# Kernel tuning notes

Measured on AMD Instinct MI355X. Metric: run time of the kernel, lower is better.

Reference implementation:

```python
import jax, jax.numpy as jnp
import numpy as np

GRID_H = 64
GRID_W = 64


def make_grid(h, w):
    # torch.meshgrid([arange(h), arange(w)], indexing='xy') -> shape (w, h);
    # grid[i, j] = (j + 0.5, i + 0.5). With h == w == 64 this is square.
    gx, gy = jnp.meshgrid(jnp.arange(h, dtype=jnp.float32),
                          jnp.arange(w, dtype=jnp.float32), indexing='xy')
    return jnp.stack([gx, gy], axis=-1) + 0.5  # (w, h, 2)


def setup_inputs() -> dict:
    key = jax.random.key(0)
    k1, k2 = jax.random.split(key)
    x = jax.random.normal(k1, (4, 128, 64, 64), dtype=jnp.float32)
    y = jax.random.normal(k2, (4, 128, 64, 64), dtype=jnp.float32)
    return {"x": x, "y": y}


def reference(x, y):
    b, c, hx, wx = x.shape
    _, _, hy, wy = y.shape
    scale = c ** (-0.5)
    grids = make_grid(GRID_H, GRID_W)[:hy, :wy].reshape(-1, 2)  # (hy*wy, 2)

    x_ = x.reshape(b, c, hx * wx)
    y_ = y.reshape(b, c, hy * wy)
    # (b, q, k) attention over all key pixels
    attn = jax.nn.softmax(jnp.einsum('bcq,bck->bqk', x_, y_) * scale, axis=-1)
    uv = jnp.einsum('bqk,kt->bqt', attn, grids)  # (b, hx*wx, 2)
    uv = uv.reshape(b, hx, wx, 2)
    # normalize to [-1, 1]
    norm = jnp.asarray([wy, hy], dtype=uv.dtype)
    uv = uv / norm * 2.0 - 1.0
    return uv
```

## Files before the change

kernel.cpp:

```cpp
#include <hip/hip_runtime.h>
#include <math.h>

typedef __attribute__((ext_vector_type(8))) _Float16 f16x8;
typedef __attribute__((ext_vector_type(4))) float f32x4;

#define NPIX 4096
#define C_DIM 128
#define SCALE 0.08838834764831845f

#define WS_NEED ((size_t)4 << 20)

__global__ __launch_bounds__(256) void conv_y(const float* __restrict__ y,
                                              char* __restrict__ ws)
{
    __shared__ float T[32][132];
    const int wg  = blockIdx.x;
    const int xcd = wg & 7;
    const int b   = xcd >> 1;
    const int sl  = ((xcd & 1) << 6) | (wg >> 3);
    const int k0  = sl * 32;
    const int t   = threadIdx.x;

    {
        const int c = t >> 1, half = t & 1;
        const float* srow = y + ((size_t)b * C_DIM + c) * NPIX + k0 + half * 16;
        float4 rv[4];
        #pragma unroll
        for (int u = 0; u < 4; ++u) rv[u] = *(const float4*)(srow + u * 4);
        #pragma unroll
        for (int u = 0; u < 4; ++u) {
            T[half * 16 + u * 4 + 0][c] = rv[u].x;
            T[half * 16 + u * 4 + 1][c] = rv[u].y;
            T[half * 16 + u * 4 + 2][c] = rv[u].z;
            T[half * 16 + u * 4 + 3][c] = rv[u].w;
        }
    }
    __syncthreads();

    char* panel = ws + (size_t)b * (NPIX * 256);
    const int k = t >> 3, g2 = t & 7;
    f16x8 v0, v1;
    #pragma unroll
    for (int m = 0; m < 8; ++m) {
        v0[m] = (_Float16)T[k][g2 * 16 + m];
        v1[m] = (_Float16)T[k][g2 * 16 + 8 + m];
    }
    const int key = k0 + k, s = key & 7;
    char* drow = panel + (size_t)key * 256;
    *(f16x8*)(drow + (((2 * g2)     ^ s) << 4)) = v0;
    *(f16x8*)(drow + (((2 * g2 + 1) ^ s) << 4)) = v1;
}

__global__ __launch_bounds__(256, 2) void uv_main(const char* __restrict__ ws,
                                                  const float* __restrict__ x,
                                                  float* __restrict__ out)
{
    __shared__ __align__(16) char Ys[2][32768];

    const int t = threadIdx.x, w = t >> 6, l = t & 63;
    const int n16 = l & 15, quad = l >> 4;
    const int wg  = blockIdx.x;
    const int xcd = wg & 7;
    const int b   = xcd >> 1;
    const int qt  = ((xcd & 1) << 6) | (wg >> 3);
    const int q0  = qt * 32;

    f16x8 bh[4][2], bl[4][2];
    {
        const float* xb = x + (size_t)b * C_DIM * NPIX + q0 + n16;
        #pragma unroll
        for (int cc = 0; cc < 4; ++cc)
            #pragma unroll
            for (int qg = 0; qg < 2; ++qg) {
                f16x8 hh, ll;
                #pragma unroll
                for (int j = 0; j < 8; ++j) {
                    const float f = xb[(size_t)(cc * 32 + quad * 8 + j) * NPIX + qg * 16] * SCALE;
                    const _Float16 fh = (_Float16)f;
                    hh[j] = fh;
                    ll[j] = (_Float16)(f - (float)fh);
                }
                bh[cc][qg] = hh;
                bl[cc][qg] = ll;
            }
    }

    const char* panel = ws + (size_t)b * (NPIX * 256);

    int aoff[2][4];
    #pragma unroll
    for (int mt = 0; mt < 2; ++mt)
        #pragma unroll
        for (int cc = 0; cc < 4; ++cc)
            aoff[mt][cc] = (mt * 64 + w * 16 + n16) * 256 + (((cc * 4 + quad) ^ (n16 & 7)) << 4);

    float gxr[4];
    #pragma unroll
    for (int r = 0; r < 4; ++r) gxr[r] = (float)(w * 16 + quad * 4 + r) + 0.5f;

    float den[2] = {0.f, 0.f}, nu[2] = {0.f, 0.f}, nv[2] = {0.f, 0.f};

    #pragma unroll
    for (int h = 0; h < 2; ++h)
        #pragma unroll
        for (int i = 0; i < 4; ++i) {
            const int off = (h * 64 + w * 16 + i * 4) * 256;
            __builtin_amdgcn_global_load_lds(
                (const __attribute__((address_space(1))) void*)(panel + off + l * 16),
                (__attribute__((address_space(3))) void*)(&Ys[0][off]), 16, 0, 0);
        }

    #pragma unroll 2
    for (int kt = 0; kt < 32; ++kt) {
        const int cur = kt & 1;
        __syncthreads();

        if (kt < 31) {
            const char* gt = panel + (size_t)(kt + 1) * 32768;
            #pragma unroll
            for (int h = 0; h < 2; ++h)
                #pragma unroll
                for (int i = 0; i < 4; ++i) {
                    const int off = (h * 64 + w * 16 + i * 4) * 256;
                    __builtin_amdgcn_global_load_lds(
                        (const __attribute__((address_space(1))) void*)(gt + off + l * 16),
                        (__attribute__((address_space(3))) void*)(&Ys[cur ^ 1][off]), 16, 0, 0);
                }
        }

        f32x4 acc[2][2];
        #pragma unroll
        for (int mt = 0; mt < 2; ++mt)
            #pragma unroll
            for (int qg = 0; qg < 2; ++qg) acc[mt][qg] = (f32x4){0.f, 0.f, 0.f, 0.f};

        #pragma unroll
        for (int cc = 0; cc < 4; ++cc) {
            const f16x8 A0 = *(const f16x8*)(&Ys[cur][aoff[0][cc]]);
            const f16x8 A1 = *(const f16x8*)(&Ys[cur][aoff[1][cc]]);
            #pragma unroll
            for (int qg = 0; qg < 2; ++qg) {
                acc[0][qg] = __builtin_amdgcn_mfma_f32_16x16x32_f16(A0, bh[cc][qg], acc[0][qg], 0, 0, 0);
                acc[0][qg] = __builtin_amdgcn_mfma_f32_16x16x32_f16(A0, bl[cc][qg], acc[0][qg], 0, 0, 0);
                acc[1][qg] = __builtin_amdgcn_mfma_f32_16x16x32_f16(A1, bh[cc][qg], acc[1][qg], 0, 0, 0);
                acc[1][qg] = __builtin_amdgcn_mfma_f32_16x16x32_f16(A1, bl[cc][qg], acc[1][qg], 0, 0, 0);
            }
        }

        #pragma unroll
        for (int qg = 0; qg < 2; ++qg) {
            float d = 0.f, u = 0.f, v = 0.f;
            #pragma unroll
            for (int mt = 0; mt < 2; ++mt) {
                const float gy = (float)(kt * 2 + mt) + 0.5f;
                #pragma unroll
                for (int r = 0; r < 4; ++r) {
                    const float p = __expf(acc[mt][qg][r]);
                    d += p;
                    u += p * gxr[r];
                    v += p * gy;
                }
            }
            den[qg] += d; nu[qg] += u; nv[qg] += v;
        }
    }

    #pragma unroll
    for (int qg = 0; qg < 2; ++qg) {
        #pragma unroll
        for (int mk = 16; mk <= 32; mk <<= 1) {
            den[qg] += __shfl_xor(den[qg], mk);
            nu[qg]  += __shfl_xor(nu[qg],  mk);
            nv[qg]  += __shfl_xor(nv[qg],  mk);
        }
    }
    __syncthreads();
    float* red = (float*)&Ys[0][0];
    if (quad == 0) {
        #pragma unroll
        for (int qg = 0; qg < 2; ++qg) {
            const int base = (w * 32 + qg * 16 + n16) * 3;
            red[base + 0] = den[qg];
            red[base + 1] = nu[qg];
            red[base + 2] = nv[qg];
        }
    }
    __syncthreads();
    if (t < 32) {
        float d = 0.f, u = 0.f, v = 0.f;
        #pragma unroll
        for (int ww = 0; ww < 4; ++ww) {
            d += red[(ww * 32 + t) * 3 + 0];
            u += red[(ww * 32 + t) * 3 + 1];
            v += red[(ww * 32 + t) * 3 + 2];
        }
        const float inv = 1.0f / d;
        *(float2*)(out + ((size_t)b * NPIX + q0 + t) * 2) =
            make_float2(u * inv * 0.03125f - 1.0f, v * inv * 0.03125f - 1.0f);
    }
}

__global__ __launch_bounds__(256, 2) void uv_attn_kernel(
    const float* __restrict__ x, const float* __restrict__ y, float* __restrict__ out)
{
    __shared__ float Xs[C_DIM][32];
    __shared__ float Ysf[64][128];
    const int tid = threadIdx.x;
    const int wgid = blockIdx.x;
    const int xcd = wgid & 7;
    const int b = xcd & 3;
    const int q0 = (((xcd >> 2) << 6) | (wgid >> 3)) * 32;
    const float* xb = x + (size_t)b * C_DIM * NPIX + q0;
    {
        const int cr = tid >> 3;
        const int cc = (tid & 7) << 2;
        #pragma unroll
        for (int i = 0; i < 4; ++i) {
            float4 v = *(const float4*)(xb + (size_t)(cr + (i << 5)) * NPIX + cc);
            v.x *= SCALE; v.y *= SCALE; v.z *= SCALE; v.w *= SCALE;
            *(float4*)(&Xs[cr + (i << 5)][cc]) = v;
        }
    }
    const int rg = tid >> 4;
    const int lane16 = tid & 15;
    const int r0 = rg << 1;
    const int col0 = lane16 << 3;
    float gxv[8];
    #pragma unroll
    for (int j2 = 0; j2 < 8; ++j2) gxv[j2] = (float)((col0 & 63) + j2) + 0.5f;
    const float gyb = (float)(lane16 >> 3) + 0.5f;
    float m_run[2] = {-INFINITY, -INFINITY};
    float den[2] = {0.f, 0.f}, nu[2] = {0.f, 0.f}, nv[2] = {0.f, 0.f};
    const int yr = tid >> 5;
    const int yc = (tid & 31) << 2;
    const float* ybase = y + (size_t)b * C_DIM * NPIX;
    for (int kt = 0; kt < 32; ++kt) {
        float S[2][8];
        #pragma unroll
        for (int r = 0; r < 2; ++r)
            #pragma unroll
            for (int j2 = 0; j2 < 8; ++j2) S[r][j2] = 0.f;
        #pragma unroll
        for (int cb = 0; cb < 2; ++cb) {
            __syncthreads();
            const float* yt = ybase + (size_t)(cb << 6) * NPIX + kt * 128;
            #pragma unroll
            for (int i = 0; i < 8; ++i)
                *(float4*)(&Ysf[yr + (i << 3)][yc]) =
                    *(const float4*)(yt + (size_t)(yr + (i << 3)) * NPIX + yc);
            __syncthreads();
            const int cbase = cb << 6;
            #pragma unroll 16
            for (int c = 0; c < 64; ++c) {
                const float2 xa = *(const float2*)(&Xs[cbase + c][r0]);
                const float4 ya = *(const float4*)(&Ysf[c][col0]);
                const float4 yb4 = *(const float4*)(&Ysf[c][col0 + 4]);
                S[0][0] += xa.x * ya.x;  S[0][1] += xa.x * ya.y;
                S[0][2] += xa.x * ya.z;  S[0][3] += xa.x * ya.w;
                S[0][4] += xa.x * yb4.x; S[0][5] += xa.x * yb4.y;
                S[0][6] += xa.x * yb4.z; S[0][7] += xa.x * yb4.w;
                S[1][0] += xa.y * ya.x;  S[1][1] += xa.y * ya.y;
                S[1][2] += xa.y * ya.z;  S[1][3] += xa.y * ya.w;
                S[1][4] += xa.y * yb4.x; S[1][5] += xa.y * yb4.y;
                S[1][6] += xa.y * yb4.z; S[1][7] += xa.y * yb4.w;
            }
        }
        const float gy = gyb + 2.0f * (float)kt;
        #pragma unroll
        for (int r = 0; r < 2; ++r) {
            float tmax = S[r][0];
            #pragma unroll
            for (int j2 = 1; j2 < 8; ++j2) tmax = fmaxf(tmax, S[r][j2]);
            #pragma unroll
            for (int mk = 8; mk >= 1; mk >>= 1) tmax = fmaxf(tmax, __shfl_xor(tmax, mk, 16));
            const float mnew = fmaxf(m_run[r], tmax);
            const float alpha = __expf(m_run[r] - mnew);
            m_run[r] = mnew;
            float psum = 0.f, pu = 0.f;
            #pragma unroll
            for (int j2 = 0; j2 < 8; ++j2) {
                const float p = __expf(S[r][j2] - mnew);
                psum += p; pu += p * gxv[j2];
            }
            den[r] = den[r] * alpha + psum;
            nu[r] = nu[r] * alpha + pu;
            nv[r] = nv[r] * alpha + gy * psum;
        }
    }
    #pragma unroll
    for (int r = 0; r < 2; ++r)
        #pragma unroll
        for (int mk = 8; mk >= 1; mk >>= 1) {
            den[r] += __shfl_xor(den[r], mk, 16);
            nu[r] += __shfl_xor(nu[r], mk, 16);
            nv[r] += __shfl_xor(nv[r], mk, 16);
        }
    if (lane16 == 0) {
        #pragma unroll
        for (int r = 0; r < 2; ++r) {
            const float inv = 1.0f / den[r];
            const int q = q0 + r0 + r;
            *(float2*)(out + ((size_t)b * NPIX + q) * 2) =
                make_float2(nu[r] * inv * 0.03125f - 1.0f, nv[r] * inv * 0.03125f - 1.0f);
        }
    }
}

extern "C" void kernel_launch(void* const* d_in, const int* in_sizes, int n_in,
                              void* d_out, int out_size, void* d_ws, size_t ws_size,
                              hipStream_t stream) {
    const float* x = (const float*)d_in[0];
    const float* y = (const float*)d_in[1];
    float* out = (float*)d_out;
    if (ws_size >= WS_NEED) {
        hipLaunchKernelGGL(conv_y, dim3(512), dim3(256), 0, stream, y, (char*)d_ws);
        hipLaunchKernelGGL(uv_main, dim3(512), dim3(256), 0, stream,
                           (const char*)d_ws, x, out);
    } else {
        hipLaunchKernelGGL(uv_attn_kernel, dim3(512), dim3(256), 0, stream, x, y, out);
    }
}
```

Measured before the change: 104.7 us.

## Switch to 32x32x16 MFMA with per-wave key rows and no block barrier

After: 107.1 us. 1.02x slower.

```diff
diff --git a/kernel.cpp b/kernel.cpp
--- a/kernel.cpp
+++ b/kernel.cpp
@@ -2,7 +2,7 @@
 #include <math.h>
 
 typedef __attribute__((ext_vector_type(8))) _Float16 f16x8;
-typedef __attribute__((ext_vector_type(4))) float f32x4;
+typedef __attribute__((ext_vector_type(16))) float f32x16;
 
 #define NPIX 4096
 #define C_DIM 128
@@ -58,132 +58,100 @@
     __shared__ __align__(16) char Ys[2][32768];
 
     const int t = threadIdx.x, w = t >> 6, l = t & 63;
-    const int n16 = l & 15, quad = l >> 4;
+    const int l32 = l & 31, h32 = l >> 5;
     const int wg  = blockIdx.x;
     const int xcd = wg & 7;
     const int b   = xcd >> 1;
     const int qt  = ((xcd & 1) << 6) | (wg >> 3);
     const int q0  = qt * 32;
 
-    f16x8 bh[4][2], bl[4][2];
+    f16x8 bh[8], bl[8];
     {
-        const float* xb = x + (size_t)b * C_DIM * NPIX + q0 + n16;
-        #pragma unroll
-        for (int cc = 0; cc < 4; ++cc)
-            #pragma unroll
-            for (int qg = 0; qg < 2; ++qg) {
-                f16x8 hh, ll;
-                #pragma unroll
-                for (int j = 0; j < 8; ++j) {
-                    const float f = xb[(size_t)(cc * 32 + quad * 8 + j) * NPIX + qg * 16] * SCALE;
-                    const _Float16 fh = (_Float16)f;
-                    hh[j] = fh;
-                    ll[j] = (_Float16)(f - (float)fh);
-                }
-                bh[cc][qg] = hh;
-                bl[cc][qg] = ll;
+        const float* xq = x + (size_t)b * C_DIM * NPIX + q0 + l32;
+        #pragma unroll
+        for (int c = 0; c < 8; ++c) {
+            f16x8 hh, ll;
+            #pragma unroll
+            for (int j = 0; j < 8; ++j) {
+                const float f = xq[(size_t)(c * 16 + h32 * 8 + j) * NPIX] * SCALE;
+                const _Float16 fh = (_Float16)f;
+                hh[j] = fh;
+                ll[j] = (_Float16)(f - (float)fh);
             }
+            bh[c] = hh;
+            bl[c] = ll;
+        }
     }
 
     const char* panel = ws + (size_t)b * (NPIX * 256);
 
-    int aoff[2][4];
-    #pragma unroll
-    for (int mt = 0; mt < 2; ++mt)
-        #pragma unroll
-        for (int cc = 0; cc < 4; ++cc)
-            aoff[mt][cc] = (mt * 64 + w * 16 + n16) * 256 + (((cc * 4 + quad) ^ (n16 & 7)) << 4);
-
-    float gxr[4];
-    #pragma unroll
-    for (int r = 0; r < 4; ++r) gxr[r] = (float)(w * 16 + quad * 4 + r) + 0.5f;
-
-    float den[2] = {0.f, 0.f}, nu[2] = {0.f, 0.f}, nv[2] = {0.f, 0.f};
-
-    #pragma unroll
-    for (int h = 0; h < 2; ++h)
-        #pragma unroll
-        for (int i = 0; i < 4; ++i) {
-            const int off = (h * 64 + w * 16 + i * 4) * 256;
-            __builtin_amdgcn_global_load_lds(
-                (const __attribute__((address_space(1))) void*)(panel + off + l * 16),
-                (__attribute__((address_space(3))) void*)(&Ys[0][off]), 16, 0, 0);
-        }
-
-    #pragma unroll 2
+    const int arow = w * 32 + l32;
+    int aoff[8];
+    #pragma unroll
+    for (int c = 0; c < 8; ++c)
+        aoff[c] = arow * 256 + (((c * 2 + h32) ^ (arow & 7)) << 4);
+
+    int soff[8];
+    #pragma unroll
+    for (int i = 0; i < 8; ++i) soff[i] = (w * 32 + i * 4) * 256 + l * 16;
+
+    #pragma unroll
+    for (int i = 0; i < 8; ++i)
+        __builtin_amdgcn_global_load_lds(
+            (const __attribute__((address_space(1))) void*)(panel + soff[i]),
+            (__attribute__((address_space(3))) void*)(&Ys[0][soff[i]]), 16, 0, 0);
+
+    const float tadd = (float)((w & 1) * 32 + 4 * h32) + 0.5f;
+    const float gyw  = (float)(w >> 1) + 0.5f;
+    float den = 0.f, nu = 0.f, nv = 0.f;
+
     for (int kt = 0; kt < 32; ++kt) {
-        const int cur = kt & 1;
-        __syncthreads();
+        char* cur = Ys[kt & 1];
+
+        __builtin_amdgcn_s_waitcnt(0x0F70 );
 
         if (kt < 31) {
             const char* gt = panel + (size_t)(kt + 1) * 32768;
-            #pragma unroll
-            for (int h = 0; h < 2; ++h)
-                #pragma unroll
-                for (int i = 0; i < 4; ++i) {
-                    const int off = (h * 64 + w * 16 + i * 4) * 256;
-                    __builtin_amdgcn_global_load_lds(
-                        (const __attribute__((address_space(1))) void*)(gt + off + l * 16),
-                        (__attribute__((address_space(3))) void*)(&Ys[cur ^ 1][off]), 16, 0, 0);
-                }
-        }
-
-        f32x4 acc[2][2];
-        #pragma unroll
-        for (int mt = 0; mt < 2; ++mt)
-            #pragma unroll
-            for (int qg = 0; qg < 2; ++qg) acc[mt][qg] = (f32x4){0.f, 0.f, 0.f, 0.f};
-
-        #pragma unroll
-        for (int cc = 0; cc < 4; ++cc) {
-            const f16x8 A0 = *(const f16x8*)(&Ys[cur][aoff[0][cc]]);
-            const f16x8 A1 = *(const f16x8*)(&Ys[cur][aoff[1][cc]]);
-            #pragma unroll
-            for (int qg = 0; qg < 2; ++qg) {
-                acc[0][qg] = __builtin_amdgcn_mfma_f32_16x16x32_f16(A0, bh[cc][qg], acc[0][qg], 0, 0, 0);
-                acc[0][qg] = __builtin_amdgcn_mfma_f32_16x16x32_f16(A0, bl[cc][qg], acc[0][qg], 0, 0, 0);
-                acc[1][qg] = __builtin_amdgcn_mfma_f32_16x16x32_f16(A1, bh[cc][qg], acc[1][qg], 0, 0, 0);
-                acc[1][qg] = __builtin_amdgcn_mfma_f32_16x16x32_f16(A1, bl[cc][qg], acc[1][qg], 0, 0, 0);
-            }
-        }
-
-        #pragma unroll
-        for (int qg = 0; qg < 2; ++qg) {
-            float d = 0.f, u = 0.f, v = 0.f;
-            #pragma unroll
-            for (int mt = 0; mt < 2; ++mt) {
-                const float gy = (float)(kt * 2 + mt) + 0.5f;
-                #pragma unroll
-                for (int r = 0; r < 4; ++r) {
-                    const float p = __expf(acc[mt][qg][r]);
-                    d += p;
-                    u += p * gxr[r];
-                    v += p * gy;
-                }
-            }
-            den[qg] += d; nu[qg] += u; nv[qg] += v;
-        }
-    }
-
-    #pragma unroll
-    for (int qg = 0; qg < 2; ++qg) {
-        #pragma unroll
-        for (int mk = 16; mk <= 32; mk <<= 1) {
-            den[qg] += __shfl_xor(den[qg], mk);
-            nu[qg]  += __shfl_xor(nu[qg],  mk);
-            nv[qg]  += __shfl_xor(nv[qg],  mk);
-        }
-    }
+            char* nb = Ys[(kt & 1) ^ 1];
+            #pragma unroll
+            for (int i = 0; i < 8; ++i)
+                __builtin_amdgcn_global_load_lds(
+                    (const __attribute__((address_space(1))) void*)(gt + soff[i]),
+                    (__attribute__((address_space(3))) void*)(&nb[soff[i]]), 16, 0, 0);
+        }
+
+        f32x16 acc = {0.f, 0.f, 0.f, 0.f, 0.f, 0.f, 0.f, 0.f,
+                      0.f, 0.f, 0.f, 0.f, 0.f, 0.f, 0.f, 0.f};
+        #pragma unroll
+        for (int c = 0; c < 8; ++c) {
+            const f16x8 A = *(const f16x8*)(cur + aoff[c]);
+            acc = __builtin_amdgcn_mfma_f32_32x32x16_f16(A, bh[c], acc, 0, 0, 0);
+            acc = __builtin_amdgcn_mfma_f32_32x32x16_f16(A, bl[c], acc, 0, 0, 0);
+        }
+
+        float ps = 0.f, pc = 0.f;
+        #pragma unroll
+        for (int r = 0; r < 16; ++r) {
+            const float p = __expf(acc[r]);
+            ps += p;
+            pc += p * (float)((r & 3) + 8 * (r >> 2));
+        }
+        den += ps;
+        nu  += pc + tadd * ps;
+        nv  += (2.0f * (float)kt + gyw) * ps;
+    }
+
+    den += __shfl_xor(den, 32);
+    nu  += __shfl_xor(nu,  32);
+    nv  += __shfl_xor(nv,  32);
+
     __syncthreads();
     float* red = (float*)&Ys[0][0];
-    if (quad == 0) {
-        #pragma unroll
-        for (int qg = 0; qg < 2; ++qg) {
-            const int base = (w * 32 + qg * 16 + n16) * 3;
-            red[base + 0] = den[qg];
-            red[base + 1] = nu[qg];
-            red[base + 2] = nv[qg];
-        }
+    if (h32 == 0) {
+        const int base = (w * 32 + l32) * 3;
+        red[base + 0] = den;
+        red[base + 1] = nu;
+        red[base + 2] = nv;
     }
     __syncthreads();
     if (t < 32) {
```
